# Performance work log

Measured on AMD Instinct MI355X. Metric: run time of the kernel, lower is better.

Reference implementation:

```python
import jax, jax.numpy as jnp
import numpy as np

EPS = 1e-5

def ste_sign(x):
    # forward: sign(x) in {-1,+1}; backward: straight-through with |x|<=1 clip
    xc = jnp.clip(x, -1.0, 1.0)
    s = jnp.where(x >= 0, 1.0, -1.0).astype(x.dtype)
    return xc + jax.lax.stop_gradient(s - xc)

def quant_w(w):
    # 1-bit weight: sign(w) scaled by mean |w| (XNOR-Net style)
    return ste_sign(w) * jnp.mean(jnp.abs(w))

def qconv(x, w, stride, pad):
    # quantized conv: binarize activations and weights, then dense conv
    xq = ste_sign(x)
    wq = quant_w(w)
    return jax.lax.conv_general_dilated(
        xq, wq, window_strides=(stride, stride),
        padding=[(pad, pad), (pad, pad)],
        dimension_numbers=('NCHW', 'OIHW', 'NCHW'))

def batchnorm(x, gamma, beta):
    # training-mode BN: batch statistics over (N, H, W)
    mu = jnp.mean(x, axis=(0, 2, 3), keepdims=True)
    var = jnp.var(x, axis=(0, 2, 3), keepdims=True)
    xhat = (x - mu) * jax.lax.rsqrt(var + EPS)
    return xhat * gamma[None, :, None, None] + beta[None, :, None, None]

def setup_inputs() -> dict:
    key = jax.random.key(0)
    ks = jax.random.split(key, 4)
    in_planes, planes = 128, 256
    x = jax.random.normal(ks[0], (64, in_planes, 56, 56), dtype=jnp.float32)
    w1 = jax.random.normal(ks[1], (planes, in_planes, 3, 3), dtype=jnp.float32) * 0.05
    w2 = jax.random.normal(ks[2], (planes, planes, 3, 3), dtype=jnp.float32) * 0.05
    ws = jax.random.normal(ks[3], (planes, in_planes, 1, 1), dtype=jnp.float32) * 0.05
    g1 = jnp.ones((planes,), jnp.float32); b1 = jnp.zeros((planes,), jnp.float32)
    g2 = jnp.ones((planes,), jnp.float32); b2 = jnp.zeros((planes,), jnp.float32)
    return {'x': x, 'w1': w1, 'g1': g1, 'b1': b1, 'w2': w2, 'g2': g2, 'b2': b2, 'ws': ws}

def reference(x, w1, g1, b1, w2, g2, b2, ws):
    out = batchnorm(qconv(x, w1, stride=2, pad=1), g1, b1)   # [N,256,28,28]
    out = qconv(out, w2, stride=1, pad=1)
    out = out + qconv(x, ws, stride=2, pad=0)                # quantized 1x1 shortcut
    out = batchnorm(out, g2, b2)
    return out
```

## Files before the change

### kernel.cpp

```cpp
#include <hip/hip_runtime.h>
#include <stdint.h>

#define N_    64
#define CIN   128
#define CMID  256
#define H_    56
#define W_    56
#define OH    28
#define OW    28
#define NPIX  (OH*OW)
#define MPAD  800
#define MTOT  (N_*MPAD)
#define CNT_CH (N_*NPIX)
#define PXH   58
#define PYH   30
#define EPS_  1e-5f

#define STATS_BYTES 16384
#define OFF_PXI 16384
#define OFF_PYI (OFF_PXI + 27551744)
#define OFF_W1F (OFF_PYI + 14745600)
#define OFF_W2F (OFF_W1F + 294912)
#define OFF_WSF (OFF_W2F + 589824)

typedef int v4i  __attribute__((ext_vector_type(4)));
typedef int v16i __attribute__((ext_vector_type(16)));

#define MFMA_I8 __builtin_amdgcn_mfma_i32_32x32x32_i8

typedef const __attribute__((address_space(1))) void* gas_t;
typedef __attribute__((address_space(3))) void* las_t;

__device__ __forceinline__ void gl_lds16(const void* g, void* l) {
  __builtin_amdgcn_global_load_lds((gas_t)g, (las_t)l, 16, 0, 0);
}

__global__ __launch_bounds__(256) void pack_x_k(const float* __restrict__ x,
                                                int8_t* __restrict__ px) {
  if (blockIdx.x >= 784) {
    int t = (blockIdx.x - 784) * 256 + threadIdx.x;
    int q = t & 7, pp = t >> 3;
    int n = pp / 228, p = pp - n * 228;
    int ih, iw;
    if (p < 58)        { ih = 0;  iw = p; }
    else if (p < 116)  { ih = 57; iw = p - 58; }
    else { int qq = p - 116; ih = 1 + (qq >> 1); iw = (qq & 1) * 57; }
    uint4* dst = (uint4*)(px + ((size_t)n * (PXH * PXH) + ih * PXH + iw) * CIN);
    dst[q] = make_uint4(0u, 0u, 0u, 0u);
    return;
  }
  int idx = blockIdx.x * 256 + threadIdx.x;
  int n = idx / (H_ * W_), hw = idx - n * (H_ * W_);
  int ih = hw / W_, iw = hw - ih * W_;
  const float* xp = x + ((size_t)n * CIN) * (H_ * W_) + hw;
  uint32_t wd[32];
#pragma unroll
  for (int c4 = 0; c4 < 32; ++c4) {
    uint32_t wv = 0u;
#pragma unroll
    for (int j = 0; j < 4; ++j) {
      uint32_t b = (xp[(size_t)(c4 * 4 + j) * (H_ * W_)] >= 0.f) ? 0x01u : 0xFFu;
      wv |= b << (j * 8);
    }
    wd[c4] = wv;
  }
  uint4* dst = (uint4*)(px + (((size_t)n * (PXH * PXH) + (ih + 1) * PXH + (iw + 1)) * CIN));
#pragma unroll
  for (int q = 0; q < 8; ++q)
    dst[q] = make_uint4(wd[q * 4], wd[q * 4 + 1], wd[q * 4 + 2], wd[q * 4 + 3]);
}

__global__ __launch_bounds__(256) void packw_all_k(const float* __restrict__ w1,
                                                   const float* __restrict__ w2,
                                                   const float* __restrict__ ws,
                                                   uint32_t* __restrict__ w1f,
                                                   uint32_t* __restrict__ w2f,
                                                   uint32_t* __restrict__ wsf,
                                                   float* __restrict__ stats) {
  int bx = blockIdx.x;
  float s = 0.f;
  if (bx < 72) {
    int T = bx * 256 + threadIdx.x;
    int l = T & 63, fb = T >> 6;
    int nb = fb & 7, kc = fb >> 3;
    int o = nb * 32 + (l & 31);
    int kbase = kc * 32 + (l >> 5) * 16;
    uint32_t wd[4] = {0u, 0u, 0u, 0u};
#pragma unroll
    for (int j = 0; j < 16; ++j) {
      int k = kbase + j, t = k >> 7, c = k & 127;
      float wv = w1[((size_t)o * CIN + c) * 9 + t];
      s += fabsf(wv);
      wd[j >> 2] |= ((wv >= 0.f) ? 0x01u : 0xFFu) << ((j & 3) * 8);
    }
    ((uint4*)w1f)[T] = make_uint4(wd[0], wd[1], wd[2], wd[3]);
    for (int off = 32; off; off >>= 1) s += __shfl_down(s, off);
    if ((threadIdx.x & 63) == 0) atomicAdd(&stats[0], s);
  } else if (bx < 216) {
    int T = (bx - 72) * 256 + threadIdx.x;
    int l = T & 63, fb = T >> 6;
    int nb = fb & 7, kc = fb >> 3;
    int o = nb * 32 + (l & 31);
    int kbase = kc * 32 + (l >> 5) * 16;
    uint32_t wd[4] = {0u, 0u, 0u, 0u};
#pragma unroll
    for (int j = 0; j < 16; ++j) {
      int k = kbase + j, t = k >> 8, c = k & 255;
      float wv = w2[((size_t)o * CMID + c) * 9 + t];
      s += fabsf(wv);
      wd[j >> 2] |= ((wv >= 0.f) ? 0x01u : 0xFFu) << ((j & 3) * 8);
    }
    ((uint4*)w2f)[T] = make_uint4(wd[0], wd[1], wd[2], wd[3]);
    for (int off = 32; off; off >>= 1) s += __shfl_down(s, off);
    if ((threadIdx.x & 63) == 0) atomicAdd(&stats[1], s);
  } else {
    int T = (bx - 216) * 256 + threadIdx.x;
    int l = T & 63, fb = T >> 6;
    int nb = fb & 7, kc = fb >> 3;
    int o = nb * 32 + (l & 31);
    int kbase = kc * 32 + (l >> 5) * 16;
    uint32_t wd[4] = {0u, 0u, 0u, 0u};
#pragma unroll
    for (int j = 0; j < 16; ++j) {
      int c = kbase + j;
      float wv = ws[(size_t)o * CIN + c];
      s += fabsf(wv);
      wd[j >> 2] |= ((wv >= 0.f) ? 0x01u : 0xFFu) << ((j & 3) * 8);
    }
    ((uint4*)wsf)[T] = make_uint4(wd[0], wd[1], wd[2], wd[3]);
    for (int off = 32; off; off >>= 1) s += __shfl_down(s, off);
    if ((threadIdx.x & 63) == 0) atomicAdd(&stats[2], s);
  }
}

__global__ __launch_bounds__(256, 2) void conv1_k(const int8_t* __restrict__ px,
                                                  const uint8_t* __restrict__ w1f,
                                                  short* __restrict__ y16,
                                                  float* __restrict__ stats) {
  __shared__ int8_t lds[2][32768];
  int bid = (blockIdx.x & 7) * 100 + (blockIdx.x >> 3);
  int bnh = bid & 1, bm = bid >> 1;
  int tid = threadIdx.x, w = tid >> 6, l = tid & 63;
  int l31 = l & 31, lhi = l >> 5;
  int blockM = bm * 128;
  int waveM = blockM + (w & 1) * 64;
  int waveN = bnh * 128 + (w >> 1) * 64;
  int nbgl2 = (w >> 1) * 2;

  int srcsw = (((l & 7) ^ (l >> 3)) << 4);
  uint32_t rowoff[4];
#pragma unroll
  for (int i = 0; i < 4; ++i) {
    int p = blockM + (w * 4 + i) * 8 + (l >> 3);
    int n = p / MPAD, hw = p - n * MPAD;
    if (hw >= NPIX) hw = 0;
    int oh = hw / OW, ow = hw - oh * OW;
    rowoff[i] = (uint32_t)((n * (PXH * PXH) + (2 * oh) * PXH + 2 * ow) * CIN);
  }
  int sw = (l31 & 7) << 4;
  uint32_t aoff[2][4];
#pragma unroll
  for (int m = 0; m < 2; ++m) {
    int pxl = (w & 1) * 64 + m * 32 + l31;
#pragma unroll
    for (int kcl = 0; kcl < 4; ++kcl)
      aoff[m][kcl] = (uint32_t)(pxl * 128 + ((kcl * 32 + lhi * 16) ^ sw));
  }

  v16i acc[2][2] = {};

  auto stage = [&](int t, int8_t* buf) {
    int kh = t / 3, kw = t - 3 * kh;
    uint32_t tapoff = (uint32_t)((kh * PXH + kw) * CIN);
#pragma unroll
    for (int i = 0; i < 4; ++i) {
      int ch = w * 4 + i;
      gl_lds16(px + (size_t)(rowoff[i] + tapoff) + srcsw, buf + ch * 1024);
      gl_lds16(w1f + ((size_t)(((t * 4 + w) * 8) + bnh * 4 + i) << 10) + l * 16,
               buf + 16384 + ch * 1024);
    }
  };

  stage(0, lds[0]);
  __syncthreads();
  for (int it = 0; it < 9; ++it) {
    if (it < 8) stage(it + 1, lds[(it + 1) & 1]);
    const int8_t* cbuf = lds[it & 1];
    v4i a[2][4], b[2][4];
#pragma unroll
    for (int m = 0; m < 2; ++m)
#pragma unroll
      for (int kcl = 0; kcl < 4; ++kcl)
        a[m][kcl] = *(const v4i*)(cbuf + aoff[m][kcl]);
#pragma unroll
    for (int n2 = 0; n2 < 2; ++n2)
#pragma unroll
      for (int kcl = 0; kcl < 4; ++kcl)
        b[n2][kcl] = *(const v4i*)(cbuf + 16384 + (kcl * 4 + nbgl2 + n2) * 1024 + l * 16);
#pragma unroll
    for (int kcl = 0; kcl < 4; ++kcl) {
      acc[0][0] = MFMA_I8(a[0][kcl], b[0][kcl], acc[0][0], 0, 0, 0);
      acc[0][1] = MFMA_I8(a[0][kcl], b[1][kcl], acc[0][1], 0, 0, 0);
      acc[1][0] = MFMA_I8(a[1][kcl], b[0][kcl], acc[1][0], 0, 0, 0);
      acc[1][1] = MFMA_I8(a[1][kcl], b[1][kcl], acc[1][1], 0, 0, 0);
    }
    __syncthreads();
  }

#pragma unroll
  for (int n2 = 0; n2 < 2; ++n2) {
    int o = waveN + n2 * 32 + l31;
    float ssum = 0.f, ssq = 0.f;
#pragma unroll
    for (int m = 0; m < 2; ++m) {
      int tbase = waveM + m * 32;
      int nb0 = tbase / MPAD, r0 = tbase - nb0 * MPAD;
#pragma unroll
      for (int r = 0; r < 16; ++r) {
        int row = (r & 3) + 8 * (r >> 2) + 4 * lhi;
        int hwr = r0 + row;
        int d = acc[m][n2][r];
        bool valid = hwr < NPIX;
        if (valid) y16[((size_t)nb0 * NPIX + hwr) * CMID + o] = (short)d;
        float fd = valid ? (float)d : 0.f;
        ssum += fd; ssq += fd * fd;
      }
    }
    ssum += __shfl_down(ssum, 32);
    ssq  += __shfl_down(ssq, 32);
    if (l < 32) { atomicAdd(&stats[16 + o], ssum); atomicAdd(&stats[272 + o], ssq); }
  }
}

__global__ __launch_bounds__(256) void pack_y_k(const short* __restrict__ y16,
                                                const float* __restrict__ stats,
                                                const float* __restrict__ g1,
                                                const float* __restrict__ b1,
                                                int8_t* __restrict__ py) {
  if (blockIdx.x >= 6272) {
    int t = (blockIdx.x - 6272) * 256 + threadIdx.x;
    int q = t & 15, pp = t >> 4;
    int n = pp / 116, p = pp - n * 116;
    int ih, iw;
    if (p < 30)       { ih = 0;  iw = p; }
    else if (p < 60)  { ih = 29; iw = p - 30; }
    else { int qq = p - 60; ih = 1 + (qq >> 1); iw = (qq & 1) * 29; }
    uint4* dst = (uint4*)(py + ((size_t)n * (PYH * PYH) + ih * PYH + iw) * CMID);
    dst[q] = make_uint4(0u, 0u, 0u, 0u);
    return;
  }
  int gid = blockIdx.x * 256 + threadIdx.x;
  int cg = gid & 31, pix = gid >> 5;
  int n = pix / NPIX, hw = pix - n * NPIX;
  int oh = hw / OW, ow = hw - oh * OW;
  uint4 raw = *(const uint4*)(y16 + (size_t)pix * CMID + cg * 8);
  float alpha1 = stats[0] * (1.f / (CMID * CIN * 9));
  float a[8], b[8];
#pragma unroll
  for (int j = 0; j < 8; ++j) {
    int c = cg * 8 + j;
    float S = stats[16 + c], S2 = stats[272 + c];
    float mu = alpha1 * (S * (1.f / CNT_CH));
    float ey2 = alpha1 * alpha1 * (S2 * (1.f / CNT_CH));
    float var = fmaxf(ey2 - mu * mu, 0.f);
    float rs = rsqrtf(var + EPS_);
    float g = g1[c];
    a[j] = g * rs * alpha1;
    b[j] = b1[c] - g * rs * mu;
  }
  int s[8];
  s[0] = (int)(short)(raw.x & 0xFFFF); s[1] = ((int)raw.x) >> 16;
  s[2] = (int)(short)(raw.y & 0xFFFF); s[3] = ((int)raw.y) >> 16;
  s[4] = (int)(short)(raw.z & 0xFFFF); s[5] = ((int)raw.z) >> 16;
  s[6] = (int)(short)(raw.w & 0xFFFF); s[7] = ((int)raw.w) >> 16;
  uint32_t w0 = 0u, w1 = 0u;
#pragma unroll
  for (int j = 0; j < 4; ++j) {
    w0 |= ((fmaf(a[j], (float)s[j], b[j]) >= 0.f) ? 0x01u : 0xFFu) << (j * 8);
    w1 |= ((fmaf(a[4 + j], (float)s[4 + j], b[4 + j]) >= 0.f) ? 0x01u : 0xFFu) << (j * 8);
  }
  size_t off = ((size_t)n * (PYH * PYH) + (oh + 1) * PYH + (ow + 1)) * CMID + cg * 8;
  *(uint2*)(py + off) = make_uint2(w0, w1);
}

__global__ __launch_bounds__(256, 2) void conv2_k(const int8_t* __restrict__ py,
                                                  const int8_t* __restrict__ px,
                                                  const uint8_t* __restrict__ w2f,
                                                  const uint8_t* __restrict__ wsf,
                                                  const float* __restrict__ stats,
                                                  float* __restrict__ out,
                                                  float* __restrict__ statw) {
  __shared__ int8_t lds[2][32768];
  int bid = (blockIdx.x & 7) * 100 + (blockIdx.x >> 3);
  int bnh = bid & 1, bm = bid >> 1;
  int tid = threadIdx.x, w = tid >> 6, l = tid & 63;
  int l31 = l & 31, lhi = l >> 5;
  int blockM = bm * 128;
  int waveM = blockM + (w & 1) * 64;
  int waveN = bnh * 128 + (w >> 1) * 64;
  int nbgl2 = (w >> 1) * 2;

  int srcsw = (((l & 7) ^ (l >> 3)) << 4);
  uint32_t rowoff[4], sxoff[4];
#pragma unroll
  for (int i = 0; i < 4; ++i) {
    int p = blockM + (w * 4 + i) * 8 + (l >> 3);
    int n = p / MPAD, hw = p - n * MPAD;
    if (hw >= NPIX) hw = 0;
    int oh = hw / OW, ow = hw - oh * OW;
    rowoff[i] = (uint32_t)((n * (PYH * PYH) + oh * PYH + ow) * CMID);
    sxoff[i]  = (uint32_t)((n * (PXH * PXH) + (2 * oh + 1) * PXH + (2 * ow + 1)) * CIN);
  }
  int sw = (l31 & 7) << 4;
  uint32_t aoff[2][4];
#pragma unroll
  for (int m = 0; m < 2; ++m) {
    int pxl = (w & 1) * 64 + m * 32 + l31;
#pragma unroll
    for (int kcl = 0; kcl < 4; ++kcl)
      aoff[m][kcl] = (uint32_t)(pxl * 128 + ((kcl * 32 + lhi * 16) ^ sw));
  }

  v16i am[2][2] = {};

  auto stageM = [&](int j, int8_t* buf) {
    int t = j >> 1, h = j & 1;
    int kh = t / 3, kw = t - 3 * kh;
    uint32_t tapoff = (uint32_t)((kh * PYH + kw) * CMID + h * 128);
    int kc = t * 8 + h * 4 + w;
#pragma unroll
    for (int i = 0; i < 4; ++i) {
      int ch = w * 4 + i;
      gl_lds16(py + (size_t)(rowoff[i] + tapoff) + srcsw, buf + ch * 1024);
      gl_lds16(w2f + ((size_t)(kc * 8 + bnh * 4 + i) << 10) + l * 16,
               buf + 16384 + ch * 1024);
    }
  };
  auto computeM = [&](const int8_t* cbuf, v16i (&ac)[2][2]) {
    v4i a[2][4], b[2][4];
#pragma unroll
    for (int m = 0; m < 2; ++m)
#pragma unroll
      for (int kcl = 0; kcl < 4; ++kcl)
        a[m][kcl] = *(const v4i*)(cbuf + aoff[m][kcl]);
#pragma unroll
    for (int n2 = 0; n2 < 2; ++n2)
#pragma unroll
      for (int kcl = 0; kcl < 4; ++kcl)
        b[n2][kcl] = *(const v4i*)(cbuf + 16384 + (kcl * 4 + nbgl2 + n2) * 1024 + l * 16);
#pragma unroll
    for (int kcl = 0; kcl < 4; ++kcl) {
      ac[0][0] = MFMA_I8(a[0][kcl], b[0][kcl], ac[0][0], 0, 0, 0);
      ac[0][1] = MFMA_I8(a[0][kcl], b[1][kcl], ac[0][1], 0, 0, 0);
      ac[1][0] = MFMA_I8(a[1][kcl], b[0][kcl], ac[1][0], 0, 0, 0);
      ac[1][1] = MFMA_I8(a[1][kcl], b[1][kcl], ac[1][1], 0, 0, 0);
    }
  };

  stageM(0, lds[0]);
  __syncthreads();
  for (int it = 0; it < 17; ++it) {
    stageM(it + 1, lds[(it + 1) & 1]);
    computeM(lds[it & 1], am);
    __syncthreads();
  }
  {
    int8_t* buf = lds[0];
#pragma unroll
    for (int i = 0; i < 4; ++i) {
      int ch = w * 4 + i;
      gl_lds16(px + (size_t)sxoff[i] + srcsw, buf + ch * 1024);
      gl_lds16(wsf + ((size_t)(w * 8 + bnh * 4 + i) << 10) + l * 16,
               buf + 16384 + ch * 1024);
    }
  }
  computeM(lds[1], am);
  __syncthreads();
  v16i as[2][2] = {};
  computeM(lds[0], as);

  float a2  = stats[1] * (1.f / (CMID * CMID * 9));
  float asx = stats[2] * (1.f / (CMID * CIN));
#pragma unroll
  for (int n2 = 0; n2 < 2; ++n2) {
    int o = waveN + n2 * 32 + l31;
    float ssum = 0.f, ssq = 0.f;
#pragma unroll
    for (int m = 0; m < 2; ++m) {
      int tbase = waveM + m * 32;
      int nb0 = tbase / MPAD, r0 = tbase - nb0 * MPAD;
#pragma unroll
      for (int r = 0; r < 16; ++r) {
        int row = (r & 3) + 8 * (r >> 2) + 4 * lhi;
        int hwr = r0 + row;
        bool valid = hwr < NPIX;
        float v = a2 * (float)am[m][n2][r] + asx * (float)as[m][n2][r];
        if (valid) out[((size_t)nb0 * CMID + o) * NPIX + hwr] = v;
        float vm = valid ? v : 0.f;
        ssum += vm; ssq += vm * vm;
      }
    }
    ssum += __shfl_down(ssum, 32);
    ssq  += __shfl_down(ssq, 32);
    if (l < 32) { atomicAdd(&statw[528 + o], ssum); atomicAdd(&statw[784 + o], ssq); }
  }
}

__global__ __launch_bounds__(256) void bn2_apply_k(float4* __restrict__ out,
                                                   const float* __restrict__ stats,
                                                   const float* __restrict__ g2,
                                                   const float* __restrict__ b2) {
  int idx = blockIdx.x * 256 + threadIdx.x;
  int c = (idx / (NPIX / 4)) & (CMID - 1);
  float S = stats[528 + c], S2 = stats[784 + c];
  float mu = S * (1.f / CNT_CH);
  float var = fmaxf(S2 * (1.f / CNT_CH) - mu * mu, 0.f);
  float rs = rsqrtf(var + EPS_);
  float g = g2[c];
  float sc = g * rs, of = b2[c] - g * rs * mu;
  float4 v = out[idx];
  v.x = v.x * sc + of; v.y = v.y * sc + of; v.z = v.z * sc + of; v.w = v.w * sc + of;
  out[idx] = v;
}

extern "C" void kernel_launch(void* const* d_in, const int* in_sizes, int n_in,
                              void* d_out, int out_size, void* d_ws, size_t ws_size,
                              hipStream_t stream) {
  const float* x   = (const float*)d_in[0];
  const float* w1  = (const float*)d_in[1];
  const float* g1  = (const float*)d_in[2];
  const float* b1  = (const float*)d_in[3];
  const float* w2  = (const float*)d_in[4];
  const float* g2  = (const float*)d_in[5];
  const float* b2  = (const float*)d_in[6];
  const float* wsc = (const float*)d_in[7];
  float* out = (float*)d_out;

  char* ws = (char*)d_ws;
  float*    stats = (float*)ws;
  int8_t*   pxi = (int8_t*)(ws + OFF_PXI);
  int8_t*   pyi = (int8_t*)(ws + OFF_PYI);
  uint32_t* w1f = (uint32_t*)(ws + OFF_W1F);
  uint32_t* w2f = (uint32_t*)(ws + OFF_W2F);
  uint32_t* wsf = (uint32_t*)(ws + OFF_WSF);
  short*    y16 = (short*)d_out;

  hipMemsetAsync(ws, 0, STATS_BYTES, stream);

  pack_x_k<<<1240, 256, 0, stream>>>(x, pxi);
  packw_all_k<<<224, 256, 0, stream>>>(w1, w2, wsc, w1f, w2f, wsf, stats);

  conv1_k<<<800, 256, 0, stream>>>(pxi, (const uint8_t*)w1f, y16, stats);
  pack_y_k<<<6736, 256, 0, stream>>>(y16, stats, g1, b1, pyi);
  conv2_k<<<800, 256, 0, stream>>>(pyi, pxi, (const uint8_t*)w2f, (const uint8_t*)wsf,
                                   stats, out, stats);
  bn2_apply_k<<<12544, 256, 0, stream>>>((float4*)out, stats, g2, b2);
}
```

Measured before the change: 340.2 us.

## Overlap global-to-LDS loads with MFMA via partial vmcnt waits; pack two pixels per thread

New measurement: 349.9 us. 1.03x slower.

```diff
diff --git a/kernel.cpp b/kernel.cpp
--- a/kernel.cpp
+++ b/kernel.cpp
@@ -35,10 +35,15 @@
   __builtin_amdgcn_global_load_lds((gas_t)g, (las_t)l, 16, 0, 0);
 }
 
+#define WAITVM8() asm volatile("s_waitcnt vmcnt(8)" ::: "memory")
+#define WAITVM0() asm volatile("s_waitcnt vmcnt(0)" ::: "memory")
+#define BAR1()    asm volatile("s_barrier" ::: "memory")
+#define BAR2()    asm volatile("s_waitcnt lgkmcnt(0)\n\ts_barrier" ::: "memory")
+
 __global__ __launch_bounds__(256) void pack_x_k(const float* __restrict__ x,
                                                 int8_t* __restrict__ px) {
-  if (blockIdx.x >= 784) {
-    int t = (blockIdx.x - 784) * 256 + threadIdx.x;
+  if (blockIdx.x >= 392) {
+    int t = (blockIdx.x - 392) * 256 + threadIdx.x;
     int q = t & 7, pp = t >> 3;
     int n = pp / 228, p = pp - n * 228;
     int ih, iw;
@@ -50,24 +55,29 @@
     return;
   }
   int idx = blockIdx.x * 256 + threadIdx.x;
-  int n = idx / (H_ * W_), hw = idx - n * (H_ * W_);
-  int ih = hw / W_, iw = hw - ih * W_;
-  const float* xp = x + ((size_t)n * CIN) * (H_ * W_) + hw;
-  uint32_t wd[32];
+  int n = idx / (H_ * 28), rem = idx - n * (H_ * 28);
+  int ih = rem / 28, p = rem - ih * 28, iw = p * 2;
+  const float* xp = x + ((size_t)n * CIN) * (H_ * W_) + ih * W_ + iw;
+  uint32_t wa[32], wb[32];
 #pragma unroll
   for (int c4 = 0; c4 < 32; ++c4) {
-    uint32_t wv = 0u;
+    uint32_t va = 0u, vb = 0u;
 #pragma unroll
     for (int j = 0; j < 4; ++j) {
-      uint32_t b = (xp[(size_t)(c4 * 4 + j) * (H_ * W_)] >= 0.f) ? 0x01u : 0xFFu;
-      wv |= b << (j * 8);
-    }
-    wd[c4] = wv;
-  }
-  uint4* dst = (uint4*)(px + (((size_t)n * (PXH * PXH) + (ih + 1) * PXH + (iw + 1)) * CIN));
-#pragma unroll
-  for (int q = 0; q < 8; ++q)
-    dst[q] = make_uint4(wd[q * 4], wd[q * 4 + 1], wd[q * 4 + 2], wd[q * 4 + 3]);
+      float2 v = *(const float2*)(xp + (size_t)(c4 * 4 + j) * (H_ * W_));
+      va |= ((v.x >= 0.f) ? 0x01u : 0xFFu) << (j * 8);
+      vb |= ((v.y >= 0.f) ? 0x01u : 0xFFu) << (j * 8);
+    }
+    wa[c4] = va; wb[c4] = vb;
+  }
+  size_t base = ((size_t)n * (PXH * PXH) + (ih + 1) * PXH + (iw + 1)) * CIN;
+  uint4* d0 = (uint4*)(px + base);
+  uint4* d1 = (uint4*)(px + base + CIN);
+#pragma unroll
+  for (int q = 0; q < 8; ++q) {
+    d0[q] = make_uint4(wa[q * 4], wa[q * 4 + 1], wa[q * 4 + 2], wa[q * 4 + 3]);
+    d1[q] = make_uint4(wb[q * 4], wb[q * 4 + 1], wb[q * 4 + 2], wb[q * 4 + 3]);
+  }
 }
 
 __global__ __launch_bounds__(256) void packw_all_k(const float* __restrict__ w1,
@@ -182,10 +192,11 @@
   };
 
   stage(0, lds[0]);
-  __syncthreads();
-  for (int it = 0; it < 9; ++it) {
-    if (it < 8) stage(it + 1, lds[(it + 1) & 1]);
-    const int8_t* cbuf = lds[it & 1];
+  for (int t = 0; t < 9; ++t) {
+    if (t < 8) { stage(t + 1, lds[(t + 1) & 1]); WAITVM8(); }
+    else       { WAITVM0(); }
+    BAR1();
+    const int8_t* cbuf = lds[t & 1];
     v4i a[2][4], b[2][4];
 #pragma unroll
     for (int m = 0; m < 2; ++m)
@@ -204,7 +215,7 @@
       acc[1][0] = MFMA_I8(a[1][kcl], b[0][kcl], acc[1][0], 0, 0, 0);
       acc[1][1] = MFMA_I8(a[1][kcl], b[1][kcl], acc[1][1], 0, 0, 0);
     }
-    __syncthreads();
+    BAR2();
   }
 
 #pragma unroll
@@ -324,16 +335,26 @@
   v16i am[2][2] = {};
 
   auto stageM = [&](int j, int8_t* buf) {
-    int t = j >> 1, h = j & 1;
-    int kh = t / 3, kw = t - 3 * kh;
-    uint32_t tapoff = (uint32_t)((kh * PYH + kw) * CMID + h * 128);
-    int kc = t * 8 + h * 4 + w;
-#pragma unroll
-    for (int i = 0; i < 4; ++i) {
-      int ch = w * 4 + i;
-      gl_lds16(py + (size_t)(rowoff[i] + tapoff) + srcsw, buf + ch * 1024);
-      gl_lds16(w2f + ((size_t)(kc * 8 + bnh * 4 + i) << 10) + l * 16,
-               buf + 16384 + ch * 1024);
+    if (j < 18) {
+      int t = j >> 1, h = j & 1;
+      int kh = t / 3, kw = t - 3 * kh;
+      uint32_t tapoff = (uint32_t)((kh * PYH + kw) * CMID + h * 128);
+      int kc = t * 8 + h * 4 + w;
+#pragma unroll
+      for (int i = 0; i < 4; ++i) {
+        int ch = w * 4 + i;
+        gl_lds16(py + (size_t)(rowoff[i] + tapoff) + srcsw, buf + ch * 1024);
+        gl_lds16(w2f + ((size_t)(kc * 8 + bnh * 4 + i) << 10) + l * 16,
+                 buf + 16384 + ch * 1024);
+      }
+    } else {
+#pragma unroll
+      for (int i = 0; i < 4; ++i) {
+        int ch = w * 4 + i;
+        gl_lds16(px + (size_t)sxoff[i] + srcsw, buf + ch * 1024);
+        gl_lds16(wsf + ((size_t)(w * 8 + bnh * 4 + i) << 10) + l * 16,
+                 buf + 16384 + ch * 1024);
+      }
     }
   };
   auto computeM = [&](const int8_t* cbuf, v16i (&ac)[2][2]) {
@@ -358,24 +379,13 @@
   };
 
   stageM(0, lds[0]);
-  __syncthreads();
-  for (int it = 0; it < 17; ++it) {
-    stageM(it + 1, lds[(it + 1) & 1]);
-    computeM(lds[it & 1], am);
-    __syncthreads();
-  }
-  {
-    int8_t* buf = lds[0];
-#pragma unroll
-    for (int i = 0; i < 4; ++i) {
-      int ch = w * 4 + i;
-      gl_lds16(px + (size_t)sxoff[i] + srcsw, buf + ch * 1024);
-      gl_lds16(wsf + ((size_t)(w * 8 + bnh * 4 + i) << 10) + l * 16,
-               buf + 16384 + ch * 1024);
-    }
-  }
-  computeM(lds[1], am);
-  __syncthreads();
+  for (int t = 0; t < 18; ++t) {
+    stageM(t + 1, lds[(t + 1) & 1]);
+    WAITVM8(); BAR1();
+    computeM(lds[t & 1], am);
+    BAR2();
+  }
+  WAITVM0(); BAR1();
   v16i as[2][2] = {};
   computeM(lds[0], as);
 
@@ -447,7 +457,7 @@
 
   hipMemsetAsync(ws, 0, STATS_BYTES, stream);
 
-  pack_x_k<<<1240, 256, 0, stream>>>(x, pxi);
+  pack_x_k<<<848, 256, 0, stream>>>(x, pxi);
   packw_all_k<<<224, 256, 0, stream>>>(w1, w2, wsc, w1f, w2f, wsf, stats);
 
   conv1_k<<<800, 256, 0, stream>>>(pxi, (const uint8_t*)w1f, y16, stats);
```
